# Kernel optimization log

Hardware: AMD Instinct MI355X
Metric: run time of the kernel (lower is better)

## Reference

```python
import jax, jax.numpy as jnp
import numpy as np

B, T, C, H = 2, 2048, 1024, 16
D = C // H  # head dim = 64


def setup_inputs() -> dict:
    key = jax.random.key(0)
    ks = jax.random.split(key, 9)
    s = 1.0 / np.sqrt(C)
    x = jax.random.normal(ks[0], (B, T, C), dtype=jnp.float32)
    # causal lower-triangular mask, broadcast over heads: [B, 1, T, T]
    attn_mask = jnp.broadcast_to(jnp.tril(jnp.ones((T, T), dtype=jnp.int32)), (B, 1, T, T))
    Wq = jax.random.normal(ks[1], (C, C), dtype=jnp.float32) * s
    Wk = jax.random.normal(ks[2], (C, C), dtype=jnp.float32) * s
    Wv = jax.random.normal(ks[3], (C, C), dtype=jnp.float32) * s
    Wo = jax.random.normal(ks[4], (C, C), dtype=jnp.float32) * s
    bq = jax.random.normal(ks[5], (C,), dtype=jnp.float32) * s
    bk = jax.random.normal(ks[6], (C,), dtype=jnp.float32) * s
    bv = jax.random.normal(ks[7], (C,), dtype=jnp.float32) * s
    bo = jax.random.normal(ks[8], (C,), dtype=jnp.float32) * s
    return {"x": x, "attn_mask": attn_mask, "Wq": Wq, "bq": bq, "Wk": Wk, "bk": bk,
            "Wv": Wv, "bv": bv, "Wo": Wo, "bo": bo}


def reference(x, attn_mask, Wq, bq, Wk, bk, Wv, bv, Wo, bo):
    # Q/K/V projections: nn.Linear applies x @ W^T + b
    def split_heads(t):  # [B,T,C] -> [B,H,T,D]
        return t.reshape(B, T, H, D).transpose(0, 2, 1, 3)

    q = split_heads(x @ Wq.T + bq)
    k = split_heads(x @ Wk.T + bk)
    v = split_heads(x @ Wv.T + bv)

    scale = 1.0 / np.sqrt(D)
    att = jnp.einsum('bhqd,bhkd->bhqk', q, k) * scale  # [B,H,T,T]
    att = jnp.where(attn_mask[:, :, :T, :T] == 0, -jnp.inf, att)
    att = jax.nn.softmax(att, axis=-1)
    # dropout p=0.0 -> identity
    y = jnp.einsum('bhqk,bhkd->bhqd', att, v)  # [B,H,T,D]
    y = y.transpose(0, 2, 1, 3).reshape(B, T, C)
    return y @ Wo.T + bo
```

## Files before the change

kernel.cpp:

```cpp
#include <hip/hip_runtime.h>
#include <hip/hip_bf16.h>

#define B_ 2
#define T_ 2048
#define C_ 1024
#define H_ 16
#define D_ 64
#define BT_ (B_ * T_)
#define S3_ 3072

typedef __bf16 bf16x8 __attribute__((ext_vector_type(8)));
typedef short short8v __attribute__((ext_vector_type(8)));
typedef short s16x4 __attribute__((ext_vector_type(4)));
typedef float f32x4 __attribute__((ext_vector_type(4)));

__device__ inline bf16x8 ld_frag_bf(const short* p) {
    short8v s = *(const short8v*)p;
    return __builtin_bit_cast(bf16x8, s);
}
__device__ inline short f2bf(float f) {
    return __builtin_bit_cast(short, (__bf16)f);
}
__device__ inline void st_out(short* p, float v) { *p = f2bf(v); }
__device__ inline void st_out(float* p, float v) { *p = v; }

__device__ inline void async16(const void* g, void* l) {
    __builtin_amdgcn_global_load_lds(
        (const __attribute__((address_space(1))) unsigned*)g,
        (__attribute__((address_space(3))) unsigned*)l, 16, 0, 0);
}

__global__ __launch_bounds__(256) void conv_inputs(
    const float* __restrict__ x,
    const float* __restrict__ Wq, const float* __restrict__ Wk,
    const float* __restrict__ Wv, const float* __restrict__ Wo,
    short* __restrict__ xb, short* __restrict__ Wqkvb, short* __restrict__ Wob)
{
    size_t e = ((size_t)blockIdx.x * 256 + threadIdx.x) * 8;
    int r = (int)(e >> 20);
    size_t off = e & ((1u << 20) - 1);
    const float* src; short* dst;
    if (r < 4)      { src = x + e;  dst = xb + e; }
    else if (r < 7) { src = (r == 4 ? Wq : r == 5 ? Wk : Wv) + off;
                      dst = Wqkvb + ((size_t)(r - 4) << 20) + off; }
    else            { src = Wo + off; dst = Wob + off; }
    f32x4 a = *(const f32x4*)src;
    f32x4 b = *(const f32x4*)(src + 4);
    short8v s;
#pragma unroll
    for (int i = 0; i < 4; ++i) { s[i] = f2bf(a[i]); s[i + 4] = f2bf(b[i]); }
    *(short8v*)dst = s;
}

__global__ __launch_bounds__(256) void gemm_qkv(
    const short* __restrict__ A,
    const short* __restrict__ Wb,
    const float* __restrict__ b0, const float* __restrict__ b1,
    const float* __restrict__ b2,
    short* __restrict__ Out, short* __restrict__ VQ)
{
    constexpr int K = 1024;
    __shared__ __align__(16) short Bs[128 * 64];
    __shared__ __align__(16) short As[128 * 64];

    const int tid = threadIdx.x;
    const int w = tid >> 6, l = tid & 63;
    const int c = l & 15, qd = l >> 4;
    const int m0 = blockIdx.y * 128, n0 = blockIdx.x * 128;
    const int wm = w >> 1, wn = w & 1;
    const int srcC = (l & 7) ^ (l >> 3);

    f32x4 acc[4][4] = {};

    for (int k0 = 0; k0 < K; k0 += 64) {
#pragma unroll
        for (int p = 0; p < 4; ++p) {
            int row = (w * 4 + p) * 8 + (l >> 3);
            async16(Wb + (size_t)(n0 + row) * K + k0 + srcC * 8,
                    Bs + (w * 4 + p) * 512 + l * 8);
            async16(A + (size_t)(m0 + row) * K + k0 + srcC * 8,
                    As + (w * 4 + p) * 512 + l * 8);
        }
        __syncthreads();

#pragma unroll
        for (int h = 0; h < 2; ++h) {
            const int slot = ((h * 4 + qd) ^ (c & 7)) * 8;
            bf16x8 af[4], bfr[4];
#pragma unroll
            for (int i = 0; i < 4; ++i) {
                af[i]  = ld_frag_bf(As + (wm * 64 + i * 16 + c) * 64 + slot);
                bfr[i] = ld_frag_bf(Bs + (wn * 64 + i * 16 + c) * 64 + slot);
            }
#pragma unroll
            for (int i = 0; i < 4; ++i)
#pragma unroll
                for (int j = 0; j < 4; ++j)
                    acc[i][j] = __builtin_amdgcn_mfma_f32_16x16x32_bf16(af[i], bfr[j], acc[i][j], 0, 0, 0);
        }
        __syncthreads();
    }

    if (n0 >= 2048) {
        const int h  = (n0 - 2048 + wn * 64) >> 6;
        const int b  = m0 >> 11;
        const int kt = ((m0 & 2047) + wm * 64) >> 6;
        short* vt = VQ + (((size_t)(b * 16 + h) * 32 + kt) * 4096);
#pragma unroll
        for (int i = 0; i < 4; ++i)
#pragma unroll
            for (int j = 0; j < 4; ++j) {
                float bv = b2[n0 - 2048 + wn * 64 + j * 16 + c];
                s16x4 st;
#pragma unroll
                for (int r = 0; r < 4; ++r) st[r] = f2bf(acc[i][j][r] + bv);
                *(s16x4*)&vt[((i * 4 + j) * 64 + qd * 16 + c) * 4] = st;
            }
    } else {
        const float* bias = (n0 < 1024) ? b0 : b1;
#pragma unroll
        for (int i = 0; i < 4; ++i)
#pragma unroll
            for (int j = 0; j < 4; ++j) {
                int n = n0 + wn * 64 + j * 16 + c;
                float bv = bias[n & 1023];
#pragma unroll
                for (int r = 0; r < 4; ++r) {
                    int m = m0 + wm * 64 + i * 16 + qd * 4 + r;
                    Out[(size_t)m * S3_ + n] = f2bf(acc[i][j][r] + bv);
                }
            }
    }
}

template <typename OT>
__global__ __launch_bounds__(256) void gemm_n64(
    const short* __restrict__ A, int lda,
    const short* __restrict__ Wb, const float* __restrict__ bias,
    OT* __restrict__ Out, int ldo)
{
    constexpr int K = 1024;
    __shared__ __align__(16) short Bs[64 * 64];
    __shared__ __align__(16) short As[128 * 64];

    const int tid = threadIdx.x;
    const int w = tid >> 6, l = tid & 63;
    const int c = l & 15, qd = l >> 4;
    const int m0 = blockIdx.y * 128, n0 = blockIdx.x * 64;
    const int wm = w >> 1, wn = w & 1;
    const int srcC = (l & 7) ^ (l >> 3);

    f32x4 acc[4][2] = {};

    for (int k0 = 0; k0 < K; k0 += 64) {
#pragma unroll
        for (int p = 0; p < 2; ++p) {
            int row = (w * 2 + p) * 8 + (l >> 3);
            async16(Wb + (size_t)(n0 + row) * K + k0 + srcC * 8,
                    Bs + (w * 2 + p) * 512 + l * 8);
        }
#pragma unroll
        for (int p = 0; p < 4; ++p) {
            int row = (w * 4 + p) * 8 + (l >> 3);
            async16(A + (size_t)(m0 + row) * lda + k0 + srcC * 8,
                    As + (w * 4 + p) * 512 + l * 8);
        }
        __syncthreads();

#pragma unroll
        for (int h = 0; h < 2; ++h) {
            const int slot = ((h * 4 + qd) ^ (c & 7)) * 8;
            bf16x8 af[4], bfr[2];
#pragma unroll
            for (int i = 0; i < 4; ++i)
                af[i] = ld_frag_bf(As + (wm * 64 + i * 16 + c) * 64 + slot);
#pragma unroll
            for (int j = 0; j < 2; ++j)
                bfr[j] = ld_frag_bf(Bs + (wn * 32 + j * 16 + c) * 64 + slot);
#pragma unroll
            for (int i = 0; i < 4; ++i)
#pragma unroll
                for (int j = 0; j < 2; ++j)
                    acc[i][j] = __builtin_amdgcn_mfma_f32_16x16x32_bf16(af[i], bfr[j], acc[i][j], 0, 0, 0);
        }
        __syncthreads();
    }

#pragma unroll
    for (int i = 0; i < 4; ++i)
#pragma unroll
        for (int j = 0; j < 2; ++j) {
            int n = n0 + wn * 32 + j * 16 + c;
            float bv = bias[n];
#pragma unroll
            for (int r = 0; r < 4; ++r) {
                int m = m0 + wm * 64 + i * 16 + qd * 4 + r;
                st_out(Out + (size_t)m * ldo + n, acc[i][j][r] + bv);
            }
        }
}

__global__ __launch_bounds__(256) void attn_flash7(
    short* __restrict__ QKV, const short* __restrict__ VQ)
{
    __shared__ __align__(16) short Ksm[2][4096];
    __shared__ __align__(16) short Vsm[2][4096];

    const int tid = threadIdx.x;
    const int w = tid >> 6, l = tid & 63;
    const int c = l & 15, qd = l >> 4;
    const int id = blockIdx.x;
    const int bh = (id & 7) * 4 + ((id >> 3) & 3);
    const int mq = id >> 5, iq = mq & 7, jq = mq >> 3;
    const int qt = jq * 8 + ((jq & 1) ? 7 - iq : iq);
    const int b = bh >> 4, h = bh & 15;
    const int sw = c & 7;

    short* Qbase = QKV + (size_t)b * T_ * S3_ + h * 64;
    const short* Kbase = Qbase + 1024;
    const short* VTb = VQ + (size_t)bh * 32 * 4096;

    const int wq0 = qt * 64 + w * 16;

    bf16x8 aq0 = ld_frag_bf(Qbase + (size_t)(wq0 + c) * S3_ + qd * 8);
    bf16x8 aq1 = ld_frag_bf(Qbase + (size_t)(wq0 + c) * S3_ + 32 + qd * 8);

    f32x4 o[4] = {};
    float lsum = 0.f;

#pragma unroll
    for (int p = 0; p < 2; ++p) {
        int row = p * 32 + w * 8 + (l >> 3);
        int srcC = (l & 7) ^ (row & 7);
        async16(Kbase + (size_t)row * S3_ + srcC * 8,
                &Ksm[0][row * 64 + (l & 7) * 8]);
        async16(VTb + p * 2048 + w * 512 + l * 8,
                &Vsm[0][p * 2048 + w * 512 + l * 8]);
    }
    __syncthreads();

#pragma unroll 1
    for (int kt = 0; kt <= qt; ++kt) {
        const int cur = kt & 1;
        const int k0 = kt * 64;

        if (kt < qt) {
            const short* vtile = VTb + (size_t)(kt + 1) * 4096;
#pragma unroll
            for (int p = 0; p < 2; ++p) {
                int row = p * 32 + w * 8 + (l >> 3);
                int srcC = (l & 7) ^ (row & 7);
                async16(Kbase + (size_t)(k0 + 64 + row) * S3_ + srcC * 8,
                        &Ksm[1 - cur][row * 64 + (l & 7) * 8]);
                async16(vtile + p * 2048 + w * 512 + l * 8,
                        &Vsm[1 - cur][p * 2048 + w * 512 + l * 8]);
            }
        }

        f32x4 st[4];
        __builtin_amdgcn_s_setprio(1);
#pragma unroll
        for (int j = 0; j < 4; ++j) {
            st[j] = (f32x4){0.f, 0.f, 0.f, 0.f};
            const short* kr = &Ksm[cur][(j * 16 + c) * 64];
            bf16x8 kb0 = ld_frag_bf(kr + (qd ^ sw) * 8);
            bf16x8 kb1 = ld_frag_bf(kr + ((qd ^ 4) ^ sw) * 8);
            st[j] = __builtin_amdgcn_mfma_f32_16x16x32_bf16(kb0, aq0, st[j], 0, 0, 0);
            st[j] = __builtin_amdgcn_mfma_f32_16x16x32_bf16(kb1, aq1, st[j], 0, 0, 0);
        }
        __builtin_amdgcn_s_setprio(0);

        s16x4 pb[4];
        if (kt < qt) {
#pragma unroll
            for (int j = 0; j < 4; ++j)
#pragma unroll
                for (int r = 0; r < 4; ++r) {
                    float p = __expf(fmaf(st[j][r], 0.125f, -8.0f));
                    lsum += p;
                    pb[j][r] = f2bf(p);
                }
        } else {
            const int qloc = w * 16 + c;
#pragma unroll
            for (int j = 0; j < 4; ++j)
#pragma unroll
                for (int r = 0; r < 4; ++r) {
                    float p = __expf(fmaf(st[j][r], 0.125f, -8.0f));
                    if (j * 16 + qd * 4 + r > qloc) p = 0.f;
                    lsum += p;
                    pb[j][r] = f2bf(p);
                }
        }

        __builtin_amdgcn_s_setprio(1);
#pragma unroll
        for (int j = 0; j < 4; ++j)
#pragma unroll
            for (int i = 0; i < 4; ++i) {
                s16x4 vf = *(const s16x4*)&Vsm[cur][((j * 4 + i) * 64 + qd * 16 + c) * 4];
                o[i] = __builtin_amdgcn_mfma_f32_16x16x16bf16_1k(vf, pb[j], o[i], 0, 0, 0);
            }
        __builtin_amdgcn_s_setprio(0);
        __syncthreads();
    }

    float lt = lsum;
    lt += __shfl_xor(lt, 16);
    lt += __shfl_xor(lt, 32);
    float inv = 1.0f / lt;

#pragma unroll
    for (int i = 0; i < 4; ++i) {
        s16x4 yb;
#pragma unroll
        for (int r = 0; r < 4; ++r) yb[r] = f2bf(o[i][r] * inv);
        *(s16x4*)&Qbase[(size_t)(wq0 + c) * S3_ + i * 16 + qd * 4] = yb;
    }
}

extern "C" void kernel_launch(void* const* d_in, const int* in_sizes, int n_in,
                              void* d_out, int out_size, void* d_ws, size_t ws_size,
                              hipStream_t stream)
{
    const float* x  = (const float*)d_in[0];
    const float* Wq = (const float*)d_in[2];
    const float* bq = (const float*)d_in[3];
    const float* Wk = (const float*)d_in[4];
    const float* bk = (const float*)d_in[5];
    const float* Wv = (const float*)d_in[6];
    const float* bv = (const float*)d_in[7];
    const float* Wo = (const float*)d_in[8];
    const float* bo = (const float*)d_in[9];
    float* out = (float*)d_out;

    short* QKVs  = (short*)d_ws;
    short* Wqkvb = QKVs + (size_t)BT_ * S3_;
    short* Wob   = Wqkvb + (size_t)S3_ * C_;
    short* xb    = (short*)d_out;
    short* VQ    = (short*)d_out + (size_t)4 * 1024 * 1024;

    conv_inputs<<<4096, 256, 0, stream>>>(x, Wq, Wk, Wv, Wo, xb, Wqkvb, Wob);
    gemm_qkv<<<dim3(S3_ / 128, BT_ / 128), 256, 0, stream>>>(
        xb, Wqkvb, bq, bk, bv, QKVs, VQ);
    attn_flash7<<<1024, 256, 0, stream>>>(QKVs, VQ);
    gemm_n64<float><<<dim3(C_ / 64, BT_ / 128), 256, 0, stream>>>(
        QKVs, S3_, Wob, bo, out, C_);
}
```

Before: 204.6 us.

## Double-buffer QKV GEMM with 256x256 tiles and 512-thread blocks

Rewrites the QKV projection GEMM to use 256x256 output tiles computed by 8 waves. The next K-tile is staged asynchronously into a second LDS buffer while MFMAs run on the current one, with the MFMA work split into quadrants and raised wave priority. The aim is to hide global-load latency and increase data reuse per tile. The cost is a much larger LDS footprint (about 128KB per block) and only 192 blocks, which may leave many CUs idle.

New measurement: 206.3 us. No clear change (+0.8%).

```diff
diff --git a/kernel.cpp b/kernel.cpp
--- a/kernel.cpp
+++ b/kernel.cpp
@@ -52,7 +52,7 @@
     *(short8v*)dst = s;
 }
 
-__global__ __launch_bounds__(256) void gemm_qkv(
+__global__ __launch_bounds__(512, 2) void gemm_qkv(
     const short* __restrict__ A,
     const short* __restrict__ Wb,
     const float* __restrict__ b0, const float* __restrict__ b1,
@@ -60,74 +60,130 @@
     short* __restrict__ Out, short* __restrict__ VQ)
 {
     constexpr int K = 1024;
-    __shared__ __align__(16) short Bs[128 * 64];
-    __shared__ __align__(16) short As[128 * 64];
+    constexpr int NT = 16;
+    __shared__ __align__(16) short As[2 * 16384];
+    __shared__ __align__(16) short Bs[2 * 16384];
 
     const int tid = threadIdx.x;
     const int w = tid >> 6, l = tid & 63;
     const int c = l & 15, qd = l >> 4;
-    const int m0 = blockIdx.y * 128, n0 = blockIdx.x * 128;
-    const int wm = w >> 1, wn = w & 1;
-    const int srcC = (l & 7) ^ (l >> 3);
-
-    f32x4 acc[4][4] = {};
-
-    for (int k0 = 0; k0 < K; k0 += 64) {
-#pragma unroll
-        for (int p = 0; p < 4; ++p) {
-            int row = (w * 4 + p) * 8 + (l >> 3);
-            async16(Wb + (size_t)(n0 + row) * K + k0 + srcC * 8,
-                    Bs + (w * 4 + p) * 512 + l * 8);
-            async16(A + (size_t)(m0 + row) * K + k0 + srcC * 8,
-                    As + (w * 4 + p) * 512 + l * 8);
-        }
-        __syncthreads();
-
-#pragma unroll
-        for (int h = 0; h < 2; ++h) {
-            const int slot = ((h * 4 + qd) ^ (c & 7)) * 8;
-            bf16x8 af[4], bfr[4];
-#pragma unroll
-            for (int i = 0; i < 4; ++i) {
-                af[i]  = ld_frag_bf(As + (wm * 64 + i * 16 + c) * 64 + slot);
-                bfr[i] = ld_frag_bf(Bs + (wn * 64 + i * 16 + c) * 64 + slot);
-            }
+    const int sw7 = c & 7;
+    const int wm = w >> 2, wn = w & 3;
+    const int m0 = blockIdx.y * 256, n0 = blockIdx.x * 256;
+
+    const int srcC = (tid & 7) ^ ((tid >> 3) & 7);
+    const int srow = tid >> 3;
+
+    f32x4 acc[8][4] = {};
+
+    auto stage_tile = [&](int slot, int t) {
+        const int k0 = t * 64;
+        short* Ad = As + slot * 16384;
+        short* Bd = Bs + slot * 16384;
+#pragma unroll
+        for (int hf = 0; hf < 2; ++hf)
+#pragma unroll
+            for (int u = 0; u < 2; ++u) {
+                int row = hf * 128 + u * 64 + srow;
+                int doff = hf * 8192 + u * 4096 + tid * 8;
+                async16(A  + (size_t)(m0 + row) * K + k0 + srcC * 8, Ad + doff);
+                async16(Wb + (size_t)(n0 + row) * K + k0 + srcC * 8, Bd + doff);
+            }
+    };
+
+    stage_tile(0, 0);
+    asm volatile("s_waitcnt vmcnt(0)" ::: "memory");
+    __builtin_amdgcn_s_barrier();
+
+    bf16x8 af[4][2], bfr[2][2];
+
+#pragma unroll 1
+    for (int t = 0; t < NT; ++t) {
+        const int p = t & 1;
+        const short* Ap = As + p * 16384;
+        const short* Bp = Bs + p * 16384;
+
+        auto LD_A = [&](int qr) {
 #pragma unroll
             for (int i = 0; i < 4; ++i)
 #pragma unroll
-                for (int j = 0; j < 4; ++j)
-                    acc[i][j] = __builtin_amdgcn_mfma_f32_16x16x32_bf16(af[i], bfr[j], acc[i][j], 0, 0, 0);
-        }
-        __syncthreads();
+                for (int h = 0; h < 2; ++h)
+                    af[i][h] = ld_frag_bf(Ap + (wm * 128 + qr * 64 + i * 16 + c) * 64
+                                             + ((h * 4 + qd) ^ sw7) * 8);
+        };
+        auto LD_B = [&](int qc) {
+#pragma unroll
+            for (int j = 0; j < 2; ++j)
+#pragma unroll
+                for (int h = 0; h < 2; ++h)
+                    bfr[j][h] = ld_frag_bf(Bp + (wn * 64 + qc * 32 + j * 16 + c) * 64
+                                              + ((h * 4 + qd) ^ sw7) * 8);
+        };
+        auto MFMA_QUAD = [&](int qr, int qc) {
+            __builtin_amdgcn_s_setprio(1);
+#pragma unroll
+            for (int i = 0; i < 4; ++i)
+#pragma unroll
+                for (int j = 0; j < 2; ++j) {
+                    f32x4 a2 = acc[qr * 4 + i][qc * 2 + j];
+                    a2 = __builtin_amdgcn_mfma_f32_16x16x32_bf16(af[i][0], bfr[j][0], a2, 0, 0, 0);
+                    a2 = __builtin_amdgcn_mfma_f32_16x16x32_bf16(af[i][1], bfr[j][1], a2, 0, 0, 0);
+                    acc[qr * 4 + i][qc * 2 + j] = a2;
+                }
+            __builtin_amdgcn_s_setprio(0);
+        };
+
+        if (t + 1 < NT) stage_tile(1 - p, t + 1);
+        LD_A(0); LD_B(0);
+        __builtin_amdgcn_s_barrier();
+        MFMA_QUAD(0, 0);
+        __builtin_amdgcn_s_barrier();
+        LD_B(1);
+        __builtin_amdgcn_s_barrier();
+        MFMA_QUAD(0, 1);
+        __builtin_amdgcn_s_barrier();
+        LD_A(1);
+        __builtin_amdgcn_s_barrier();
+        MFMA_QUAD(1, 1);
+        __builtin_amdgcn_s_barrier();
+        LD_B(0);
+        __builtin_amdgcn_s_barrier();
+        MFMA_QUAD(1, 0);
+        if (t + 1 < NT)
+            asm volatile("s_waitcnt vmcnt(0)" ::: "memory");
+        __builtin_amdgcn_s_barrier();
     }
 
     if (n0 >= 2048) {
-        const int h  = (n0 - 2048 + wn * 64) >> 6;
-        const int b  = m0 >> 11;
-        const int kt = ((m0 & 2047) + wm * 64) >> 6;
-        short* vt = VQ + (((size_t)(b * 16 + h) * 32 + kt) * 4096);
-#pragma unroll
-        for (int i = 0; i < 4; ++i)
-#pragma unroll
-            for (int j = 0; j < 4; ++j) {
-                float bv = b2[n0 - 2048 + wn * 64 + j * 16 + c];
+        const int h = ((n0 - 2048) >> 6) + wn;
+        const int b = m0 >> 11;
+        const int base_kt = (m0 & 2047) >> 6;
+#pragma unroll
+        for (int ai = 0; ai < 8; ++ai) {
+            const int kt = base_kt + wm * 2 + (ai >> 2);
+            const int ik = ai & 3;
+            short* vt = VQ + (((size_t)(b * 16 + h) * 32 + kt) * 4096);
+#pragma unroll
+            for (int aj = 0; aj < 4; ++aj) {
+                float bv = b2[(n0 - 2048) + wn * 64 + aj * 16 + c];
                 s16x4 st;
 #pragma unroll
-                for (int r = 0; r < 4; ++r) st[r] = f2bf(acc[i][j][r] + bv);
-                *(s16x4*)&vt[((i * 4 + j) * 64 + qd * 16 + c) * 4] = st;
-            }
+                for (int r = 0; r < 4; ++r) st[r] = f2bf(acc[ai][aj][r] + bv);
+                *(s16x4*)&vt[((ik * 4 + aj) * 64 + qd * 16 + c) * 4] = st;
+            }
+        }
     } else {
         const float* bias = (n0 < 1024) ? b0 : b1;
 #pragma unroll
-        for (int i = 0; i < 4; ++i)
-#pragma unroll
-            for (int j = 0; j < 4; ++j) {
-                int n = n0 + wn * 64 + j * 16 + c;
+        for (int ai = 0; ai < 8; ++ai)
+#pragma unroll
+            for (int aj = 0; aj < 4; ++aj) {
+                int n = n0 + wn * 64 + aj * 16 + c;
                 float bv = bias[n & 1023];
 #pragma unroll
                 for (int r = 0; r < 4; ++r) {
-                    int m = m0 + wm * 64 + i * 16 + qd * 4 + r;
-                    Out[(size_t)m * S3_ + n] = f2bf(acc[i][j][r] + bv);
+                    int m = m0 + wm * 128 + ai * 16 + qd * 4 + r;
+                    Out[(size_t)m * S3_ + n] = f2bf(acc[ai][aj][r] + bv);
                 }
             }
     }
@@ -341,7 +397,7 @@
     short* VQ    = (short*)d_out + (size_t)4 * 1024 * 1024;
 
     conv_inputs<<<4096, 256, 0, stream>>>(x, Wq, Wk, Wv, Wo, xb, Wqkvb, Wob);
-    gemm_qkv<<<dim3(S3_ / 128, BT_ / 128), 256, 0, stream>>>(
+    gemm_qkv<<<dim3(S3_ / 256, BT_ / 256), 512, 0, stream>>>(
         xb, Wqkvb, bq, bk, bv, QKVs, VQ);
     attn_flash7<<<1024, 256, 0, stream>>>(QKVs, VQ);
     gemm_n64<float><<<dim3(C_ / 64, BT_ / 128), 256, 0, stream>>>(
```
